# Performance work log

Measured on AMD Instinct MI355X. Metric: run time of the kernel, lower is better.

Reference implementation:

```python
import jax, jax.numpy as jnp
import numpy as np

D_MODEL = 1024
NUM_HEADS = 16
HEAD_DIM = D_MODEL // NUM_HEADS


def setup_inputs() -> dict:
    key = jax.random.key(0)
    k1, k2, k3 = jax.random.split(key, 3)
    B, T = 4, 2048
    x = jax.random.normal(k1, (B, T, D_MODEL), dtype=jnp.float32)
    # nn.Linear weights: out = x @ W.T; store torch-layout [out_features, in_features]
    w_qkv = jax.random.normal(k2, (3 * D_MODEL, D_MODEL), dtype=jnp.float32) * (D_MODEL ** -0.5)
    w_proj = jax.random.normal(k3, (D_MODEL, D_MODEL), dtype=jnp.float32) * (D_MODEL ** -0.5)
    return {"x": x, "w_qkv": w_qkv, "w_proj": w_proj}


def reference(x, w_qkv, w_proj):
    B, T, C = x.shape
    H, Dh = NUM_HEADS, HEAD_DIM
    qkv = jnp.einsum('btc,fc->btf', x, w_qkv)          # [B,T,3C]
    q, k, v = jnp.split(qkv, 3, axis=2)
    # [B,T,C] -> [B,H,T,Dh]
    q = q.reshape(B, T, H, Dh).transpose(0, 2, 1, 3)
    k = k.reshape(B, T, H, Dh).transpose(0, 2, 1, 3)
    v = v.reshape(B, T, H, Dh).transpose(0, 2, 1, 3)
    scale = Dh ** -0.5
    att = jnp.einsum('bhqd,bhkd->bhqk', q, k) * scale  # [B,H,T,T]
    causal = jnp.tril(jnp.ones((T, T), dtype=bool))
    att = jnp.where(causal, att, -jnp.inf)
    att = jax.nn.softmax(att, axis=-1)
    y = jnp.einsum('bhqk,bhkd->bhqd', att, v)          # [B,H,T,Dh]
    y = y.transpose(0, 2, 1, 3).reshape(B, T, C)
    return jnp.einsum('btc,oc->bto', y, w_proj)
```

## Files before the change

kernel.cpp:

```cpp
#include <hip/hip_runtime.h>
#include <stdint.h>
#include <math.h>

typedef __bf16 bf16;
typedef __bf16 bf16x4 __attribute__((ext_vector_type(4)));
typedef __bf16 bf16x8 __attribute__((ext_vector_type(8)));
typedef float f32x4 __attribute__((ext_vector_type(4)));

#define MFMA16(a, b, c) __builtin_amdgcn_mfma_f32_16x16x32_bf16((a), (b), (c), 0, 0, 0)

typedef __attribute__((address_space(1))) void* as1v;
typedef __attribute__((address_space(3))) void* as3v;

__device__ __forceinline__ void async_ld16(const void* g, void* l) {
  __builtin_amdgcn_global_load_lds((as1v)(uintptr_t)g,
                                   (as3v)(unsigned int)(uintptr_t)l, 16, 0, 0);
}

__global__ __launch_bounds__(256) void cast3_k(const float* __restrict__ x,
                                               const float* __restrict__ wq,
                                               const float* __restrict__ wp,
                                               bf16* __restrict__ xb,
                                               bf16* __restrict__ wqb,
                                               bf16* __restrict__ wpb) {
  const long i = (long)blockIdx.x * 256 + threadIdx.x;
  const float4* src;
  bf16x4* dst;
  long off;
  if (i < 2097152L) {
    src = (const float4*)x;  dst = (bf16x4*)xb;  off = i;
  } else if (i < 2097152L + 786432L) {
    src = (const float4*)wq; dst = (bf16x4*)wqb; off = i - 2097152L;
  } else {
    src = (const float4*)wp; dst = (bf16x4*)wpb; off = i - 2097152L - 786432L;
  }
  float4 v = src[off];
  bf16x4 o;
  o[0] = (bf16)v.x; o[1] = (bf16)v.y; o[2] = (bf16)v.z; o[3] = (bf16)v.w;
  dst[off] = o;
}

__global__ __launch_bounds__(256, 2) void gemm_qkv(const bf16* __restrict__ A,
                                                   const bf16* __restrict__ Bm,
                                                   bf16* __restrict__ qb,
                                                   bf16* __restrict__ kb,
                                                   bf16* __restrict__ vth) {
  __shared__ bf16 As[2][128 * 64];
  __shared__ bf16 Bs[2][192 * 64];
  const int tid  = threadIdx.x;
  const int lane = tid & 63;
  const int wv   = tid >> 6;
  const int wm   = wv >> 1;
  const int wn   = wv & 1;
  const int lr   = lane & 15;
  const int quad = lane >> 4;
  const long m0 = (long)blockIdx.y * 128;
  const long n0 = (long)blockIdx.x * 192;

  const int srow = lane >> 3;
  const int scg  = (lane & 7) ^ srow;
  const int swz  = lr & 7;

  const f32x4 fz = {0.f, 0.f, 0.f, 0.f};
  f32x4 acc[4][6];
#pragma unroll
  for (int i = 0; i < 4; ++i)
#pragma unroll
    for (int j = 0; j < 6; ++j) acc[i][j] = fz;

#define STAGE_QKV(kt, bufi)                                                        \
  do {                                                                             \
    const long kk = (long)(kt) * 64;                                               \
    _Pragma("unroll") for (int i_ = 0; i_ < 4; ++i_)                               \
        async_ld16(&A[(m0 + i_ * 32 + wv * 8 + srow) * 1024 + kk + scg * 8],       \
                   &As[bufi][(i_ * 32 + wv * 8) * 64]);                            \
    _Pragma("unroll") for (int i_ = 0; i_ < 6; ++i_)                               \
        async_ld16(&Bm[(n0 + i_ * 32 + wv * 8 + srow) * 1024 + kk + scg * 8],      \
                   &Bs[bufi][(i_ * 32 + wv * 8) * 64]);                            \
  } while (0)

  STAGE_QKV(0, 0);

#pragma unroll 2
  for (int t = 0; t < 16; ++t) {
    const int cur = t & 1;
    if (t < 15) {
      STAGE_QKV(t + 1, cur ^ 1);
      asm volatile("s_waitcnt vmcnt(10)" ::: "memory");
    } else {
      asm volatile("s_waitcnt vmcnt(0)" ::: "memory");
    }
    __builtin_amdgcn_s_barrier();

    bf16x8 af[2][4], bfr[2][6];
#pragma unroll
    for (int ds = 0; ds < 2; ++ds) {
      const int slot = ((ds << 2) + quad) ^ swz;
#pragma unroll
      for (int mi = 0; mi < 4; ++mi)
        af[ds][mi] = *(const bf16x8*)&As[cur][(wm * 64 + mi * 16 + lr) * 64 + slot * 8];
#pragma unroll
      for (int ni = 0; ni < 6; ++ni)
        bfr[ds][ni] = *(const bf16x8*)&Bs[cur][(wn * 96 + ni * 16 + lr) * 64 + slot * 8];
    }
#pragma unroll
    for (int ds = 0; ds < 2; ++ds)
#pragma unroll
      for (int mi = 0; mi < 4; ++mi)
#pragma unroll
        for (int ni = 0; ni < 6; ++ni)
          acc[mi][ni] = MFMA16(af[ds][mi], bfr[ds][ni], acc[mi][ni]);

    if (t < 15) __builtin_amdgcn_s_barrier();
  }
#undef STAGE_QKV

  const float kS = 0.18033688f;
#pragma unroll
  for (int mi = 0; mi < 4; ++mi) {
    const long row = m0 + wm * 64 + mi * 16 + quad * 4;
#pragma unroll
    for (int ni = 0; ni < 6; ++ni) {
      const long col = n0 + wn * 96 + ni * 16 + lr;
      if (col < 1024) {
#pragma unroll
        for (int r = 0; r < 4; ++r) qb[(row + r) * 1024 + col] = (bf16)(acc[mi][ni][r] * kS);
      } else if (col < 2048) {
        const long kc = col - 1024;
#pragma unroll
        for (int r = 0; r < 4; ++r) kb[(row + r) * 1024 + kc] = (bf16)(acc[mi][ni][r]);
      } else {
        const long vcol = col - 2048;
        const long h = vcol >> 6, d = vcol & 63;
        const long b = row >> 11;
        const long tt = row & 2047;
        bf16x4 pk;
#pragma unroll
        for (int r = 0; r < 4; ++r) pk[r] = (bf16)(acc[mi][ni][r]);
        *(bf16x4*)&vth[(((b << 4) + h) * 64 + d) * 2048 + tt] = pk;
      }
    }
  }
}

__global__ __launch_bounds__(256, 2) void gemm_proj(const bf16* __restrict__ A,
                                                    const bf16* __restrict__ Bm,
                                                    float* __restrict__ C) {
  __shared__ bf16 As[2][128 * 64];
  __shared__ bf16 Bs[2][128 * 64];
  const int tid  = threadIdx.x;
  const int lane = tid & 63;
  const int wv   = tid >> 6;
  const int wm   = wv >> 1;
  const int wn   = wv & 1;
  const int lr   = lane & 15;
  const int quad = lane >> 4;
  const long m0 = (long)blockIdx.y * 128;
  const long n0 = (long)blockIdx.x * 128;

  const int srow = lane >> 3;
  const int scg  = (lane & 7) ^ srow;
  const int swz  = lr & 7;

  const f32x4 fz = {0.f, 0.f, 0.f, 0.f};
  f32x4 acc[4][4];
#pragma unroll
  for (int i = 0; i < 4; ++i)
#pragma unroll
    for (int j = 0; j < 4; ++j) acc[i][j] = fz;

#define STAGE_PROJ(kt, bufi)                                                       \
  do {                                                                             \
    const long kk = (long)(kt) * 64;                                               \
    _Pragma("unroll") for (int i_ = 0; i_ < 4; ++i_) {                             \
      const int rb = i_ * 32 + wv * 8;                                             \
      async_ld16(&A[(m0 + rb + srow) * 1024 + kk + scg * 8], &As[bufi][rb * 64]);  \
      async_ld16(&Bm[(n0 + rb + srow) * 1024 + kk + scg * 8], &Bs[bufi][rb * 64]); \
    }                                                                              \
  } while (0)

  STAGE_PROJ(0, 0);

#pragma unroll 2
  for (int t = 0; t < 16; ++t) {
    const int cur = t & 1;
    if (t < 15) {
      STAGE_PROJ(t + 1, cur ^ 1);
      asm volatile("s_waitcnt vmcnt(8)" ::: "memory");
    } else {
      asm volatile("s_waitcnt vmcnt(0)" ::: "memory");
    }
    __builtin_amdgcn_s_barrier();

    bf16x8 af[2][4], bfr[2][4];
#pragma unroll
    for (int ds = 0; ds < 2; ++ds) {
      const int slot = ((ds << 2) + quad) ^ swz;
#pragma unroll
      for (int mi = 0; mi < 4; ++mi)
        af[ds][mi] = *(const bf16x8*)&As[cur][(wm * 64 + mi * 16 + lr) * 64 + slot * 8];
#pragma unroll
      for (int ni = 0; ni < 4; ++ni)
        bfr[ds][ni] = *(const bf16x8*)&Bs[cur][(wn * 64 + ni * 16 + lr) * 64 + slot * 8];
    }
#pragma unroll
    for (int ds = 0; ds < 2; ++ds)
#pragma unroll
      for (int mi = 0; mi < 4; ++mi)
#pragma unroll
        for (int ni = 0; ni < 4; ++ni)
          acc[mi][ni] = MFMA16(af[ds][mi], bfr[ds][ni], acc[mi][ni]);

    if (t < 15) __builtin_amdgcn_s_barrier();
  }
#undef STAGE_PROJ

#pragma unroll
  for (int mi = 0; mi < 4; ++mi) {
    const long row = m0 + wm * 64 + mi * 16 + quad * 4;
#pragma unroll
    for (int ni = 0; ni < 4; ++ni) {
      const long col = n0 + wn * 64 + ni * 16 + lr;
#pragma unroll
      for (int r = 0; r < 4; ++r) C[(row + r) * 1024 + col] = acc[mi][ni][r];
    }
  }
}

__global__ __launch_bounds__(256, 2) void flash_attn10(const bf16* __restrict__ q,
                                                       const bf16* __restrict__ k,
                                                       const bf16* __restrict__ vth,
                                                       bf16* __restrict__ y) {
  __shared__ bf16 Ks[2][64 * 64];
  __shared__ bf16 Vt[2][64 * 64];
  __shared__ bf16 Ps[4][32 * 72];
  const int tid  = threadIdx.x;
  const int lane = tid & 63;
  const int wv   = tid >> 6;
  const int lr   = lane & 15;
  const int quad = lane >> 4;
  const int lin  = blockIdx.x + (blockIdx.y << 3);
  const int xcd  = lin & 7;
  const int slot = lin >> 3;
  const int p    = slot & 7;
  const int bh   = ((slot >> 3) << 3) | xcd;
  const int b = bh >> 4, h = bh & 15;
  const bf16* qp = q + ((size_t)b * 2048) * 1024 + h * 64;
  const bf16* kp = k + ((size_t)b * 2048) * 1024 + h * 64;
  const bf16* vp = vth + (size_t)bh * 64 * 2048;
  bf16* yp = y + ((size_t)b * 2048) * 1024 + h * 64;

  const int stg_row = lane >> 3;
  const int stg_cg  = (lane & 7) ^ stg_row;
  const int swz     = lr & 7;

  bf16x8 ones;
#pragma unroll
  for (int j = 0; j < 8; ++j) ones[j] = (bf16)1.0f;
  const f32x4 fz = {0.f, 0.f, 0.f, 0.f};

  for (int half = 0; half < 2; ++half) {
    const int qt = half ? p : 15 - p;
    const int q0 = qt * 128;
    const int kb_max = 2 * qt + 1;
    const int kmax_w = 2 * qt + (wv >> 1);

    bf16x8 qf[2][2];
#pragma unroll
    for (int nq = 0; nq < 2; ++nq) {
      const int qrow = q0 + wv * 32 + nq * 16 + lr;
#pragma unroll
      for (int ds = 0; ds < 2; ++ds)
        qf[nq][ds] = *(const bf16x8*)(qp + (size_t)qrow * 1024 + ds * 32 + quad * 8);
    }

    f32x4 o[2][4];
    f32x4 lacc[2];
#pragma unroll
    for (int nq = 0; nq < 2; ++nq) {
      lacc[nq] = fz;
#pragma unroll
      for (int nf = 0; nf < 4; ++nf) o[nq][nf] = fz;
    }

#pragma unroll
    for (int i = 0; i < 2; ++i) {
      const int r = i * 32 + wv * 8 + stg_row;
      async_ld16(vp + (size_t)r * 2048 + stg_cg * 8, &Vt[0][(i * 32 + wv * 8) * 64]);
      async_ld16(kp + (size_t)r * 1024 + stg_cg * 8, &Ks[0][(i * 32 + wv * 8) * 64]);
    }

    for (int kt = 0; kt <= kb_max; ++kt) {
      const int k0 = kt * 64;
      const int cb = kt & 1;
      asm volatile("s_waitcnt vmcnt(0)" ::: "memory");
      __builtin_amdgcn_s_barrier();

      if (kt < kb_max) {
        const int k1 = k0 + 64;
#pragma unroll
        for (int i = 0; i < 2; ++i) {
          const int r = i * 32 + wv * 8 + stg_row;
          async_ld16(vp + (size_t)r * 2048 + k1 + stg_cg * 8,
                     &Vt[cb ^ 1][(i * 32 + wv * 8) * 64]);
          async_ld16(kp + (size_t)(k1 + r) * 1024 + stg_cg * 8,
                     &Ks[cb ^ 1][(i * 32 + wv * 8) * 64]);
        }
      }

      if (kt <= kmax_w) {
        f32x4 s[2][4];
#pragma unroll
        for (int nq = 0; nq < 2; ++nq)
#pragma unroll
          for (int mi = 0; mi < 4; ++mi) s[nq][mi] = fz;
#pragma unroll
        for (int ds = 0; ds < 2; ++ds)
#pragma unroll
          for (int mi = 0; mi < 4; ++mi) {
            const bf16x8 ak =
                *(const bf16x8*)&Ks[cb][(mi * 16 + lr) * 64 + (((ds << 2) + quad) ^ swz) * 8];
            s[0][mi] = MFMA16(ak, qf[0][ds], s[0][mi]);
            s[1][mi] = MFMA16(ak, qf[1][ds], s[1][mi]);
          }

        if (kt < kmax_w) {
#pragma unroll
          for (int nq = 0; nq < 2; ++nq) {
            const int qloc = nq * 16 + lr;
#pragma unroll
            for (int mi = 0; mi < 4; ++mi) {
              bf16x4 pb;
#pragma unroll
              for (int r = 0; r < 4; ++r) pb[r] = (bf16)__builtin_amdgcn_exp2f(s[nq][mi][r]);
              *(bf16x4*)&Ps[wv][qloc * 72 + mi * 16 + quad * 4] = pb;
            }
          }
        } else {
          const int kofs = k0 - q0 - wv * 32;
#pragma unroll
          for (int nq = 0; nq < 2; ++nq) {
            const int qloc = nq * 16 + lr;
#pragma unroll
            for (int mi = 0; mi < 4; ++mi) {
              bf16x4 pb;
#pragma unroll
              for (int r = 0; r < 4; ++r) {
                float pv = __builtin_amdgcn_exp2f(s[nq][mi][r]);
                if (mi * 16 + quad * 4 + r + kofs > qloc) pv = 0.0f;
                pb[r] = (bf16)pv;
              }
              *(bf16x4*)&Ps[wv][qloc * 72 + mi * 16 + quad * 4] = pb;
            }
          }
        }

        bf16x8 ap[2][2];
#pragma unroll
        for (int ks = 0; ks < 2; ++ks) {
          ap[0][ks] = *(const bf16x8*)&Ps[wv][(lr) * 72 + ks * 32 + quad * 8];
          ap[1][ks] = *(const bf16x8*)&Ps[wv][(16 + lr) * 72 + ks * 32 + quad * 8];
        }
#pragma unroll
        for (int ks = 0; ks < 2; ++ks) {
          lacc[0] = MFMA16(ap[0][ks], ones, lacc[0]);
          lacc[1] = MFMA16(ap[1][ks], ones, lacc[1]);
#pragma unroll
          for (int nf = 0; nf < 4; ++nf) {
            const bf16x8 bv =
                *(const bf16x8*)&Vt[cb][(nf * 16 + lr) * 64 + (((ks << 2) + quad) ^ swz) * 8];
            o[0][nf] = MFMA16(ap[0][ks], bv, o[0][nf]);
            o[1][nf] = MFMA16(ap[1][ks], bv, o[1][nf]);
          }
        }
      }
    }

#pragma unroll
    for (int nq = 0; nq < 2; ++nq)
#pragma unroll
      for (int r = 0; r < 4; ++r) {
        const float inv = __builtin_amdgcn_rcpf(lacc[nq][r]);
        const int t = q0 + wv * 32 + nq * 16 + quad * 4 + r;
#pragma unroll
        for (int nf = 0; nf < 4; ++nf)
          yp[(size_t)t * 1024 + nf * 16 + lr] = (bf16)(o[nq][nf][r] * inv);
      }
  }
}

extern "C" void kernel_launch(void* const* d_in, const int* in_sizes, int n_in,
                              void* d_out, int out_size, void* d_ws, size_t ws_size,
                              hipStream_t stream) {
  const float* x      = (const float*)d_in[0];
  const float* w_qkv  = (const float*)d_in[1];
  const float* w_proj = (const float*)d_in[2];
  float* out = (float*)d_out;
  char* ws = (char*)d_ws;

  bf16* xb   = (bf16*)(ws);
  bf16* wqkb = (bf16*)(ws + (16ull << 20));
  bf16* wpb  = (bf16*)(ws + (22ull << 20));
  bf16* qb   = (bf16*)(ws + (24ull << 20));
  bf16* kbuf = (bf16*)(ws + (40ull << 20));
  bf16* vth  = (bf16*)(ws + (56ull << 20));
  bf16* yb   = (bf16*)(ws + (72ull << 20));

  cast3_k<<<dim3(12288), 256, 0, stream>>>(x, w_qkv, w_proj, xb, wqkb, wpb);
  gemm_qkv<<<dim3(16, 64), 256, 0, stream>>>(xb, wqkb, qb, kbuf, vth);
  flash_attn10<<<dim3(8, 64), 256, 0, stream>>>(qb, kbuf, vth, yb);
  gemm_proj<<<dim3(8, 64), 256, 0, stream>>>(yb, wpb, out);
}
```

Baseline: 221.5 us.

## Enlarge QKV GEMM tile to 256x192 with 8 waves and interleaved prefetch

The QKV projection GEMM now uses 512-thread blocks that compute a 256x192 output tile, half as many blocks as before. Each of the 8 waves computes 128x48 instead of 64x96. Next-stage global-to-LDS loads are split into chunks issued between MFMA groups, with partial vmcnt waits, and s_setprio is raised around the MFMA clusters. The aim is better reuse of each B tile and better overlap of loads with math. In exchange it needs more LDS per block and has fewer blocks to spread over the CUs.

New measurement: 226.2 us. 2.2% more time.

```diff
diff --git a/kernel.cpp b/kernel.cpp
--- a/kernel.cpp
+++ b/kernel.cpp
@@ -40,21 +40,21 @@
   dst[off] = o;
 }
 
-__global__ __launch_bounds__(256, 2) void gemm_qkv(const bf16* __restrict__ A,
+__global__ __launch_bounds__(512, 2) void gemm_qkv(const bf16* __restrict__ A,
                                                    const bf16* __restrict__ Bm,
                                                    bf16* __restrict__ qb,
                                                    bf16* __restrict__ kb,
                                                    bf16* __restrict__ vth) {
-  __shared__ bf16 As[2][128 * 64];
+  __shared__ bf16 As[2][256 * 64];
   __shared__ bf16 Bs[2][192 * 64];
   const int tid  = threadIdx.x;
   const int lane = tid & 63;
   const int wv   = tid >> 6;
-  const int wm   = wv >> 1;
-  const int wn   = wv & 1;
+  const int wm   = wv >> 2;
+  const int wn   = wv & 3;
   const int lr   = lane & 15;
   const int quad = lane >> 4;
-  const long m0 = (long)blockIdx.y * 128;
+  const long m0 = (long)blockIdx.y * 256;
   const long n0 = (long)blockIdx.x * 192;
 
   const int srow = lane >> 3;
@@ -62,66 +62,83 @@
   const int swz  = lr & 7;
 
   const f32x4 fz = {0.f, 0.f, 0.f, 0.f};
-  f32x4 acc[4][6];
-#pragma unroll
-  for (int i = 0; i < 4; ++i)
-#pragma unroll
-    for (int j = 0; j < 6; ++j) acc[i][j] = fz;
-
-#define STAGE_QKV(kt, bufi)                                                        \
-  do {                                                                             \
-    const long kk = (long)(kt) * 64;                                               \
-    _Pragma("unroll") for (int i_ = 0; i_ < 4; ++i_)                               \
-        async_ld16(&A[(m0 + i_ * 32 + wv * 8 + srow) * 1024 + kk + scg * 8],       \
-                   &As[bufi][(i_ * 32 + wv * 8) * 64]);                            \
-    _Pragma("unroll") for (int i_ = 0; i_ < 6; ++i_)                               \
-        async_ld16(&Bm[(n0 + i_ * 32 + wv * 8 + srow) * 1024 + kk + scg * 8],      \
-                   &Bs[bufi][(i_ * 32 + wv * 8) * 64]);                            \
-  } while (0)
-
-  STAGE_QKV(0, 0);
+  f32x4 acc[8][3];
+#pragma unroll
+  for (int i = 0; i < 8; ++i)
+#pragma unroll
+    for (int j = 0; j < 3; ++j) acc[i][j] = fz;
+
+#define LD_A(kt, bufi, j)                                                           \
+  async_ld16(&A[(m0 + (j) * 64 + wv * 8 + srow) * 1024 + (long)(kt) * 64 + scg * 8], \
+             &As[bufi][((j) * 64 + wv * 8) * 64])
+#define LD_B(kt, bufi, j)                                                           \
+  async_ld16(&Bm[(n0 + (j) * 64 + wv * 8 + srow) * 1024 + (long)(kt) * 64 + scg * 8],\
+             &Bs[bufi][((j) * 64 + wv * 8) * 64])
+
+  LD_A(0, 0, 0); LD_A(0, 0, 1); LD_A(0, 0, 2); LD_A(0, 0, 3);
+  LD_B(0, 0, 0); LD_B(0, 0, 1); LD_B(0, 0, 2);
+  LD_A(1, 1, 0); LD_A(1, 1, 1);
+  asm volatile("s_waitcnt vmcnt(2)" ::: "memory");
+  __builtin_amdgcn_s_barrier();
 
 #pragma unroll 2
   for (int t = 0; t < 16; ++t) {
-    const int cur = t & 1;
+    const int cur = t & 1, nxt = cur ^ 1;
+
+    bf16x8 bfr[3][2];
+#pragma unroll
+    for (int ni = 0; ni < 3; ++ni)
+#pragma unroll
+      for (int ks = 0; ks < 2; ++ks)
+        bfr[ni][ks] = *(const bf16x8*)
+            &Bs[cur][(wn * 48 + ni * 16 + lr) * 64 + (((ks << 2) + quad) ^ swz) * 8];
+
+#pragma unroll
+    for (int q = 0; q < 4; ++q) {
+      if (t < 15) {
+        if (q == 0) { LD_A(t + 1, nxt, 2); LD_A(t + 1, nxt, 3); }
+        if (q == 1) { LD_B(t + 1, nxt, 0); LD_B(t + 1, nxt, 1); }
+        if (q == 2) { LD_B(t + 1, nxt, 2); }
+      }
+      bf16x8 af[2][2];
+#pragma unroll
+      for (int m2 = 0; m2 < 2; ++m2)
+#pragma unroll
+        for (int ks = 0; ks < 2; ++ks)
+          af[m2][ks] = *(const bf16x8*)
+              &As[cur][(wm * 128 + (q * 2 + m2) * 16 + lr) * 64 + (((ks << 2) + quad) ^ swz) * 8];
+      __builtin_amdgcn_s_setprio(1);
+#pragma unroll
+      for (int m2 = 0; m2 < 2; ++m2)
+#pragma unroll
+        for (int ni = 0; ni < 3; ++ni)
+#pragma unroll
+          for (int ks = 0; ks < 2; ++ks)
+            acc[q * 2 + m2][ni] = MFMA16(af[m2][ks], bfr[ni][ks], acc[q * 2 + m2][ni]);
+      __builtin_amdgcn_s_setprio(0);
+    }
+
+    if (t < 14) {
+      asm volatile("s_waitcnt lgkmcnt(0)" ::: "memory");
+      __builtin_amdgcn_s_barrier();
+      LD_A(t + 2, cur, 0); LD_A(t + 2, cur, 1);
+    }
     if (t < 15) {
-      STAGE_QKV(t + 1, cur ^ 1);
-      asm volatile("s_waitcnt vmcnt(10)" ::: "memory");
-    } else {
-      asm volatile("s_waitcnt vmcnt(0)" ::: "memory");
-    }
-    __builtin_amdgcn_s_barrier();
-
-    bf16x8 af[2][4], bfr[2][6];
-#pragma unroll
-    for (int ds = 0; ds < 2; ++ds) {
-      const int slot = ((ds << 2) + quad) ^ swz;
-#pragma unroll
-      for (int mi = 0; mi < 4; ++mi)
-        af[ds][mi] = *(const bf16x8*)&As[cur][(wm * 64 + mi * 16 + lr) * 64 + slot * 8];
-#pragma unroll
-      for (int ni = 0; ni < 6; ++ni)
-        bfr[ds][ni] = *(const bf16x8*)&Bs[cur][(wn * 96 + ni * 16 + lr) * 64 + slot * 8];
-    }
-#pragma unroll
-    for (int ds = 0; ds < 2; ++ds)
-#pragma unroll
-      for (int mi = 0; mi < 4; ++mi)
-#pragma unroll
-        for (int ni = 0; ni < 6; ++ni)
-          acc[mi][ni] = MFMA16(af[ds][mi], bfr[ds][ni], acc[mi][ni]);
-
-    if (t < 15) __builtin_amdgcn_s_barrier();
-  }
-#undef STAGE_QKV
+      if (t < 14) asm volatile("s_waitcnt vmcnt(2)" ::: "memory");
+      else        asm volatile("s_waitcnt vmcnt(0)" ::: "memory");
+      __builtin_amdgcn_s_barrier();
+    }
+  }
+#undef LD_A
+#undef LD_B
 
   const float kS = 0.18033688f;
 #pragma unroll
-  for (int mi = 0; mi < 4; ++mi) {
-    const long row = m0 + wm * 64 + mi * 16 + quad * 4;
-#pragma unroll
-    for (int ni = 0; ni < 6; ++ni) {
-      const long col = n0 + wn * 96 + ni * 16 + lr;
+  for (int mi = 0; mi < 8; ++mi) {
+    const long row = m0 + wm * 128 + mi * 16 + quad * 4;
+#pragma unroll
+    for (int ni = 0; ni < 3; ++ni) {
+      const long col = n0 + wn * 48 + ni * 16 + lr;
       if (col < 1024) {
 #pragma unroll
         for (int r = 0; r < 4; ++r) qb[(row + r) * 1024 + col] = (bf16)(acc[mi][ni][r] * kS);
@@ -407,7 +424,7 @@
   bf16* yb   = (bf16*)(ws + (72ull << 20));
 
   cast3_k<<<dim3(12288), 256, 0, stream>>>(x, w_qkv, w_proj, xb, wqkb, wpb);
-  gemm_qkv<<<dim3(16, 64), 256, 0, stream>>>(xb, wqkb, qb, kbuf, vth);
+  gemm_qkv<<<dim3(16, 32), 512, 0, stream>>>(xb, wqkb, qb, kbuf, vth);
   flash_attn10<<<dim3(8, 64), 256, 0, stream>>>(qb, kbuf, vth, yb);
   gemm_proj<<<dim3(8, 64), 256, 0, stream>>>(yb, wpb, out);
 }
```

## Software-pipeline PV matmul one tile behind QK in flash attention

Applied to the files above, without the earlier changes.

Restructures the attention inner loop so each iteration computes QK^T and softmax for the current key tile while doing the P·V product for the previous tile, using a triple-buffered V tile in shared memory and ping-pong P fragments in registers. A final P·V step after the loop drains the pipeline. The aim is to hide the exp/LDS-write/LDS-read latency of P behind MFMA work. In exchange it uses more LDS and registers, which may affect occupancy at 2 blocks per CU, and adds a barrier per half.

New measurement: 277.4 us. +25.2%, slower.

```diff
diff --git a/kernel.cpp b/kernel.cpp
--- a/kernel.cpp
+++ b/kernel.cpp
@@ -227,12 +227,12 @@
   }
 }
 
-__global__ __launch_bounds__(256, 2) void flash_attn10(const bf16* __restrict__ q,
+__global__ __launch_bounds__(256, 2) void flash_attn11(const bf16* __restrict__ q,
                                                        const bf16* __restrict__ k,
                                                        const bf16* __restrict__ vth,
                                                        bf16* __restrict__ y) {
   __shared__ bf16 Ks[2][64 * 64];
-  __shared__ bf16 Vt[2][64 * 64];
+  __shared__ bf16 Vt[3][64 * 64];
   __shared__ bf16 Ps[4][32 * 72];
   const int tid  = threadIdx.x;
   const int lane = tid & 63;
@@ -265,6 +265,8 @@
     const int kb_max = 2 * qt + 1;
     const int kmax_w = 2 * qt + (wv >> 1);
 
+    __syncthreads();
+
     bf16x8 qf[2][2];
 #pragma unroll
     for (int nq = 0; nq < 2; ++nq) {
@@ -282,6 +284,8 @@
 #pragma unroll
       for (int nf = 0; nf < 4; ++nf) o[nq][nf] = fz;
     }
+
+    bf16x8 apA[2][2], apB[2][2];
 
 #pragma unroll
     for (int i = 0; i < 2; ++i) {
@@ -290,90 +294,104 @@
       async_ld16(kp + (size_t)r * 1024 + stg_cg * 8, &Ks[0][(i * 32 + wv * 8) * 64]);
     }
 
+#define FBODY(APC, APP)                                                              \
+  do {                                                                               \
+    f32x4 s[2][4];                                                                   \
+    if (act) {                                                                       \
+      _Pragma("unroll") for (int nq = 0; nq < 2; ++nq)                               \
+        _Pragma("unroll") for (int mi = 0; mi < 4; ++mi) s[nq][mi] = fz;             \
+      _Pragma("unroll") for (int ds = 0; ds < 2; ++ds)                               \
+        _Pragma("unroll") for (int mi = 0; mi < 4; ++mi) {                           \
+          const bf16x8 ak = *(const bf16x8*)&Ks[cb][(mi * 16 + lr) * 64 +            \
+                                                    (((ds << 2) + quad) ^ swz) * 8]; \
+          s[0][mi] = MFMA16(ak, qf[0][ds], s[0][mi]);                                \
+          s[1][mi] = MFMA16(ak, qf[1][ds], s[1][mi]);                                \
+        }                                                                            \
+    }                                                                                \
+    if (pact) {             \
+      _Pragma("unroll") for (int ks = 0; ks < 2; ++ks)                               \
+        _Pragma("unroll") for (int nf = 0; nf < 4; ++nf) {                           \
+          const bf16x8 bv = *(const bf16x8*)&Vt[vprev][(nf * 16 + lr) * 64 +         \
+                                                      (((ks << 2) + quad) ^ swz) * 8]; \
+          o[0][nf] = MFMA16(APP[0][ks], bv, o[0][nf]);                               \
+          o[1][nf] = MFMA16(APP[1][ks], bv, o[1][nf]);                               \
+        }                                                                            \
+    }                                                                                \
+    if (act) {                                                                       \
+      if (kt < kmax_w) {                                                             \
+        _Pragma("unroll") for (int nq = 0; nq < 2; ++nq) {                           \
+          const int qloc = nq * 16 + lr;                                             \
+          _Pragma("unroll") for (int mi = 0; mi < 4; ++mi) {                         \
+            bf16x4 pb;                                                               \
+            _Pragma("unroll") for (int r = 0; r < 4; ++r)                            \
+                pb[r] = (bf16)__builtin_amdgcn_exp2f(s[nq][mi][r]);                  \
+            *(bf16x4*)&Ps[wv][qloc * 72 + mi * 16 + quad * 4] = pb;                  \
+          }                                                                          \
+        }                                                                            \
+      } else {                                                                       \
+        const int kofs = k0 - q0 - wv * 32;                                          \
+        _Pragma("unroll") for (int nq = 0; nq < 2; ++nq) {                           \
+          const int qloc = nq * 16 + lr;                                             \
+          _Pragma("unroll") for (int mi = 0; mi < 4; ++mi) {                         \
+            bf16x4 pb;                                                               \
+            _Pragma("unroll") for (int r = 0; r < 4; ++r) {                          \
+              float pv2 = __builtin_amdgcn_exp2f(s[nq][mi][r]);                      \
+              if (mi * 16 + quad * 4 + r + kofs > qloc) pv2 = 0.0f;                  \
+              pb[r] = (bf16)pv2;                                                     \
+            }                                                                        \
+            *(bf16x4*)&Ps[wv][qloc * 72 + mi * 16 + quad * 4] = pb;                  \
+          }                                                                          \
+        }                                                                            \
+      }                                                                              \
+      _Pragma("unroll") for (int ks = 0; ks < 2; ++ks) {                             \
+        APC[0][ks] = *(const bf16x8*)&Ps[wv][(lr) * 72 + ks * 32 + quad * 8];        \
+        APC[1][ks] = *(const bf16x8*)&Ps[wv][(16 + lr) * 72 + ks * 32 + quad * 8];   \
+      }                                                                              \
+      _Pragma("unroll") for (int ks = 0; ks < 2; ++ks) {                             \
+        lacc[0] = MFMA16(APC[0][ks], ones, lacc[0]);                                 \
+        lacc[1] = MFMA16(APC[1][ks], ones, lacc[1]);                                 \
+      }                                                                              \
+    }                                                                                \
+  } while (0)
+
     for (int kt = 0; kt <= kb_max; ++kt) {
       const int k0 = kt * 64;
       const int cb = kt & 1;
+      const int vprev = (kt + 2) % 3;
       asm volatile("s_waitcnt vmcnt(0)" ::: "memory");
       __builtin_amdgcn_s_barrier();
 
       if (kt < kb_max) {
         const int k1 = k0 + 64;
+        const int vnext = (kt + 1) % 3;
 #pragma unroll
         for (int i = 0; i < 2; ++i) {
           const int r = i * 32 + wv * 8 + stg_row;
           async_ld16(vp + (size_t)r * 2048 + k1 + stg_cg * 8,
-                     &Vt[cb ^ 1][(i * 32 + wv * 8) * 64]);
+                     &Vt[vnext][(i * 32 + wv * 8) * 64]);
           async_ld16(kp + (size_t)(k1 + r) * 1024 + stg_cg * 8,
                      &Ks[cb ^ 1][(i * 32 + wv * 8) * 64]);
         }
       }
 
-      if (kt <= kmax_w) {
-        f32x4 s[2][4];
-#pragma unroll
-        for (int nq = 0; nq < 2; ++nq)
-#pragma unroll
-          for (int mi = 0; mi < 4; ++mi) s[nq][mi] = fz;
-#pragma unroll
-        for (int ds = 0; ds < 2; ++ds)
-#pragma unroll
-          for (int mi = 0; mi < 4; ++mi) {
-            const bf16x8 ak =
-                *(const bf16x8*)&Ks[cb][(mi * 16 + lr) * 64 + (((ds << 2) + quad) ^ swz) * 8];
-            s[0][mi] = MFMA16(ak, qf[0][ds], s[0][mi]);
-            s[1][mi] = MFMA16(ak, qf[1][ds], s[1][mi]);
-          }
-
-        if (kt < kmax_w) {
-#pragma unroll
-          for (int nq = 0; nq < 2; ++nq) {
-            const int qloc = nq * 16 + lr;
-#pragma unroll
-            for (int mi = 0; mi < 4; ++mi) {
-              bf16x4 pb;
-#pragma unroll
-              for (int r = 0; r < 4; ++r) pb[r] = (bf16)__builtin_amdgcn_exp2f(s[nq][mi][r]);
-              *(bf16x4*)&Ps[wv][qloc * 72 + mi * 16 + quad * 4] = pb;
-            }
-          }
-        } else {
-          const int kofs = k0 - q0 - wv * 32;
-#pragma unroll
-          for (int nq = 0; nq < 2; ++nq) {
-            const int qloc = nq * 16 + lr;
-#pragma unroll
-            for (int mi = 0; mi < 4; ++mi) {
-              bf16x4 pb;
-#pragma unroll
-              for (int r = 0; r < 4; ++r) {
-                float pv = __builtin_amdgcn_exp2f(s[nq][mi][r]);
-                if (mi * 16 + quad * 4 + r + kofs > qloc) pv = 0.0f;
-                pb[r] = (bf16)pv;
-              }
-              *(bf16x4*)&Ps[wv][qloc * 72 + mi * 16 + quad * 4] = pb;
-            }
-          }
+      const bool act  = (kt <= kmax_w);
+      const bool pact = (kt > 0) && (kt - 1 <= kmax_w);
+      if (kt & 1) FBODY(apB, apA);
+      else        FBODY(apA, apB);
+    }
+#undef FBODY
+
+    if (kb_max <= kmax_w) {
+      const int vlast = kb_max % 3;
+#pragma unroll
+      for (int ks = 0; ks < 2; ++ks)
+#pragma unroll
+        for (int nf = 0; nf < 4; ++nf) {
+          const bf16x8 bv = *(const bf16x8*)&Vt[vlast][(nf * 16 + lr) * 64 +
+                                                      (((ks << 2) + quad) ^ swz) * 8];
+          o[0][nf] = MFMA16(apB[0][ks], bv, o[0][nf]);
+          o[1][nf] = MFMA16(apB[1][ks], bv, o[1][nf]);
         }
-
-        bf16x8 ap[2][2];
-#pragma unroll
-        for (int ks = 0; ks < 2; ++ks) {
-          ap[0][ks] = *(const bf16x8*)&Ps[wv][(lr) * 72 + ks * 32 + quad * 8];
-          ap[1][ks] = *(const bf16x8*)&Ps[wv][(16 + lr) * 72 + ks * 32 + quad * 8];
-        }
-#pragma unroll
-        for (int ks = 0; ks < 2; ++ks) {
-          lacc[0] = MFMA16(ap[0][ks], ones, lacc[0]);
-          lacc[1] = MFMA16(ap[1][ks], ones, lacc[1]);
-#pragma unroll
-          for (int nf = 0; nf < 4; ++nf) {
-            const bf16x8 bv =
-                *(const bf16x8*)&Vt[cb][(nf * 16 + lr) * 64 + (((ks << 2) + quad) ^ swz) * 8];
-            o[0][nf] = MFMA16(ap[0][ks], bv, o[0][nf]);
-            o[1][nf] = MFMA16(ap[1][ks], bv, o[1][nf]);
-          }
-        }
-      }
     }
 
 #pragma unroll
@@ -408,6 +426,6 @@
 
   cast3_k<<<dim3(12288), 256, 0, stream>>>(x, w_qkv, w_proj, xb, wqkb, wpb);
   gemm_qkv<<<dim3(16, 64), 256, 0, stream>>>(xb, wqkb, qb, kbuf, vth);
-  flash_attn10<<<dim3(8, 64), 256, 0, stream>>>(qb, kbuf, vth, yb);
+  flash_attn11<<<dim3(8, 64), 256, 0, stream>>>(qb, kbuf, vth, yb);
   gemm_proj<<<dim3(8, 64), 256, 0, stream>>>(yb, wpb, out);
 }
```
